# Performance work log

Measured on AMD Instinct MI355X. Metric: run time of the kernel, lower is better.

The kernel has to match this reference:

```python
import jax, jax.numpy as jnp
import numpy as np

VOCAB, EMBED, HIDDEN, LAYERS = 128, 256, 512, 2
B, T = 64, 512


def setup_inputs() -> dict:
    key = jax.random.key(0)
    ks = jax.random.split(key, 10)
    x = jax.random.randint(ks[0], (B, T), 0, VOCAB)
    emb = jax.random.normal(ks[1], (VOCAB, EMBED), jnp.float32) * 0.02
    emb = emb.at[0].set(0.0)  # padding_idx=0
    inp = {"x": x, "embedding": emb}
    in_dims = [EMBED, HIDDEN]
    for l in range(LAYERS):
        s = 1.0 / np.sqrt(in_dims[l])
        inp[f"W_xh{l}"] = jax.random.uniform(ks[2 + 3 * l], (HIDDEN, in_dims[l]), jnp.float32, -s, s)
        # orthogonal-ish init for W_hh
        a = jax.random.normal(ks[3 + 3 * l], (HIDDEN, HIDDEN), jnp.float32)
        q, _ = jnp.linalg.qr(a)
        inp[f"W_hh{l}"] = q
        inp[f"b_h{l}"] = jnp.zeros((HIDDEN,), jnp.float32)
    s = 1.0 / np.sqrt(HIDDEN)
    inp["W_hy"] = jax.random.uniform(ks[8], (VOCAB, HIDDEN), jnp.float32, -s, s)
    inp["b_y"] = jax.random.uniform(ks[9], (VOCAB,), jnp.float32, -s, s)
    return inp


def _rnn_layer(layer_in, W_xh, W_hh, b_h):
    # layer_in: (B, T, D). Precompute input projection for all t, scan recurrence.
    xW = jnp.einsum('btd,hd->bth', layer_in, W_xh) + b_h  # (B, T, H)
    h0 = jnp.zeros((layer_in.shape[0], W_hh.shape[0]), layer_in.dtype)

    def step(h_prev, xW_t):
        h_t = jnp.tanh(xW_t + h_prev @ W_hh.T)
        return h_t, h_t

    h_last, hs = jax.lax.scan(step, h0, jnp.swapaxes(xW, 0, 1))  # hs: (T, B, H)
    return jnp.swapaxes(hs, 0, 1), h_last


def reference(x, embedding, W_xh0, W_hh0, b_h0, W_xh1, W_hh1, b_h1, W_hy, b_y):
    layer_in = embedding[x]  # (B, T, E)
    hidden = []
    for W_xh, W_hh, b_h in ((W_xh0, W_hh0, b_h0), (W_xh1, W_hh1, b_h1)):
        layer_in, h_last = _rnn_layer(layer_in, W_xh, W_hh, b_h)
        hidden.append(h_last)
    logits = jnp.einsum('bth,vh->btv', layer_in, W_hy) + b_y
    return (logits, *hidden)
```

## Files before the change

### kernel.cpp

```cpp
#include <hip/hip_runtime.h>
#include <hip/hip_fp16.h>

typedef _Float16 f16x8 __attribute__((ext_vector_type(8)));
typedef float f32x4 __attribute__((ext_vector_type(4)));
typedef unsigned int u32x4 __attribute__((ext_vector_type(4)));
typedef unsigned int u32x2 __attribute__((ext_vector_type(2)));
typedef unsigned long long u64;

static constexpr int T_SEQ = 512;
static constexpr int BATCH = 64;
static constexpr int HID   = 512;
static constexpr int VOC   = 128;

static constexpr int AOFF_EMB  = 0;
static constexpr int AOFF_WXH0 = 32768;
static constexpr int AOFF_WHH0 = 163840;
static constexpr int AOFF_WXH1 = 425984;
static constexpr int AOFF_WHH1 = 688128;
static constexpr int AOFF_WHY  = 950272;
static constexpr int ATOT      = 1015808;

static constexpr size_t OFF_RING   = 16384;
static constexpr size_t RING_BYTES = 32ull * 4 * 512 * 16;
static constexpr size_t OFF_HIST   = OFF_RING + RING_BYTES;
static constexpr size_t HIST_BYTES = 512ull * 16 * 512 * 16;
static constexpr size_t OFF_ARENA  = OFF_HIST + HIST_BYTES;
static constexpr size_t OFF_XW0    = OFF_ARENA + 2ull * ATOT;
static constexpr size_t PLANE_B    = (size_t)T_SEQ * BATCH * HID * 2;
static constexpr size_t OFF_H1A    = OFF_XW0 + PLANE_B;

__device__ __forceinline__ unsigned short h2u(_Float16 h) {
  union { _Float16 h; unsigned short u; } c; c.h = h; return c.u;
}
__device__ __forceinline__ _Float16 u2h(unsigned short u) {
  union { unsigned short u; _Float16 h; } c; c.u = u; return c.h;
}
__device__ __forceinline__ float fast_tanh(float x) {
  float e = __expf(2.0f * x);
  return 1.0f - 2.0f * __builtin_amdgcn_rcpf(e + 1.0f);
}

__device__ __forceinline__ void store16_sys(u64* addr, u64 data, unsigned tag) {
  u32x4 v;
  v.x = (unsigned)data; v.y = (unsigned)(data >> 32);
  v.z = tag;            v.w = 0u;
  asm volatile("global_store_dwordx4 %0, %1, off sc0 sc1"
               :: "v"(addr), "v"(v) : "memory");
}
__device__ __forceinline__ void issue3x16(const u64* a, const u64* b, const u64* c,
                                          u32x4& v0, u32x4& v1, u32x4& v2) {
  asm volatile("global_load_dwordx4 %0, %3, off sc0 sc1\n\t"
               "global_load_dwordx4 %1, %4, off sc0 sc1\n\t"
               "global_load_dwordx4 %2, %5, off sc0 sc1"
               : "=&v"(v0), "=&v"(v1), "=&v"(v2)
               : "v"(a), "v"(b), "v"(c)
               : "memory");
}
__device__ __forceinline__ void issue4x16(const u64* a, const u64* b, const u64* c,
                                          const u64* d, u32x4& v0, u32x4& v1,
                                          u32x4& v2, u32x4& v3) {
  asm volatile("global_load_dwordx4 %0, %4, off sc0 sc1\n\t"
               "global_load_dwordx4 %1, %5, off sc0 sc1\n\t"
               "global_load_dwordx4 %2, %6, off sc0 sc1\n\t"
               "global_load_dwordx4 %3, %7, off sc0 sc1"
               : "=&v"(v0), "=&v"(v1), "=&v"(v2), "=&v"(v3)
               : "v"(a), "v"(b), "v"(c), "v"(d)
               : "memory");
}
__device__ __forceinline__ void wait3(u32x4& v0, u32x4& v1, u32x4& v2) {
  asm volatile("s_waitcnt vmcnt(0)" : "+v"(v0), "+v"(v1), "+v"(v2) :: "memory");
}
__device__ __forceinline__ void wait4_v3(u32x4& v0, u32x4& v1, u32x4& v2, u32x4& v3) {
  asm volatile("s_waitcnt vmcnt(3)" : "+v"(v0), "+v"(v1), "+v"(v2), "+v"(v3) :: "memory");
}
__device__ __forceinline__ void wait4_v0(u32x4& v0, u32x4& v1, u32x4& v2, u32x4& v3) {
  asm volatile("s_waitcnt vmcnt(0)" : "+v"(v0), "+v"(v1), "+v"(v2), "+v"(v3) :: "memory");
}
__device__ __forceinline__ void load3x16_sys(const u64* a, const u64* b, const u64* c,
                                             u32x4& v0, u32x4& v1, u32x4& v2) {
  asm volatile("global_load_dwordx4 %0, %3, off sc0 sc1\n\t"
               "global_load_dwordx4 %1, %4, off sc0 sc1\n\t"
               "global_load_dwordx4 %2, %5, off sc0 sc1\n\t"
               "s_waitcnt vmcnt(0)"
               : "=&v"(v0), "=&v"(v1), "=&v"(v2)
               : "v"(a), "v"(b), "v"(c)
               : "memory");
}
__device__ __forceinline__ void load4x16_sys(const u64* a, const u64* b, const u64* c,
                                             const u64* d, u32x4& v0, u32x4& v1,
                                             u32x4& v2, u32x4& v3) {
  asm volatile("global_load_dwordx4 %0, %4, off sc0 sc1\n\t"
               "global_load_dwordx4 %1, %5, off sc0 sc1\n\t"
               "global_load_dwordx4 %2, %6, off sc0 sc1\n\t"
               "global_load_dwordx4 %3, %7, off sc0 sc1\n\t"
               "s_waitcnt vmcnt(0)"
               : "=&v"(v0), "=&v"(v1), "=&v"(v2), "=&v"(v3)
               : "v"(a), "v"(b), "v"(c), "v"(d)
               : "memory");
}

__global__ __launch_bounds__(256) void canon_kernel(
    const float* p0, const float* p1, const float* p2, const float* p3,
    const float* p4, const float* p5, _Float16* __restrict__ dst,
    int* __restrict__ ringhist) {
  const int NZ = (int)((RING_BYTES + HIST_BYTES) / 4);
  for (int i = blockIdx.x * 256 + threadIdx.x; i < NZ; i += gridDim.x * 256)
    ringhist[i] = 0;
  const float* srcs[6] = {p0, p1, p2, p3, p4, p5};
  const int ns[6] = {32768, 131072, 262144, 262144, 262144, 65536};
  for (int i = blockIdx.x * 256 + threadIdx.x; i < ATOT; i += gridDim.x * 256) {
    int off = i, s = 0;
    while (off >= ns[s]) { off -= ns[s]; ++s; }
    dst[i] = (_Float16)srcs[s][off];
  }
}

__global__ __launch_bounds__(256) void xw0_kernel(
    const int* __restrict__ x, const _Float16* __restrict__ emb,
    const _Float16* __restrict__ Wxh, const float* __restrict__ bh,
    _Float16* __restrict__ xwf) {
  __shared__ _Float16 Bs[64][264];
  const int t = blockIdx.x, n0 = blockIdx.y * 64, tid = threadIdx.x;
#pragma unroll
  for (int rep = 0; rep < 8; ++rep) {
    int flat = rep * 256 + tid;
    int row = flat >> 5, c8 = flat & 31;
    *(f16x8*)&Bs[row][c8 * 8] = *(const f16x8*)&Wxh[(size_t)(n0 + row) * 256 + c8 * 8];
  }
  __syncthreads();
  const int wv = tid >> 6, lane = tid & 63, l15 = lane & 15, quad = lane >> 4;
  const int b = wv * 16 + l15;
  const int idx = x[b * 512 + t];
  f32x4 acc[4];
#pragma unroll
  for (int nt = 0; nt < 4; ++nt) { float bv = bh[n0 + nt * 16 + l15]; acc[nt] = {bv, bv, bv, bv}; }
#pragma unroll
  for (int kc = 0; kc < 8; ++kc) {
    f16x8 a = *(const f16x8*)&emb[(size_t)idx * 256 + kc * 32 + quad * 8];
#pragma unroll
    for (int nt = 0; nt < 4; ++nt) {
      f16x8 bf = *(const f16x8*)&Bs[nt * 16 + l15][kc * 32 + quad * 8];
      acc[nt] = __builtin_amdgcn_mfma_f32_16x16x32_f16(a, bf, acc[nt], 0, 0, 0);
    }
  }
#pragma unroll
  for (int nt = 0; nt < 4; ++nt) {
    unsigned int lo = (unsigned int)h2u((_Float16)acc[nt][0]) |
                      ((unsigned int)h2u((_Float16)acc[nt][1]) << 16);
    unsigned int hi = (unsigned int)h2u((_Float16)acc[nt][2]) |
                      ((unsigned int)h2u((_Float16)acc[nt][3]) << 16);
    u32x2 pk = {lo, hi};
    *(u32x2*)&xwf[(size_t)t * 32768 + (size_t)(n0 + nt * 16 + l15) * 64 + wv * 16 + quad * 4] = pk;
  }
}

__device__ __forceinline__ void layer0_loop(
    const _Float16* __restrict__ Whh, const _Float16* __restrict__ xwf,
    u64* __restrict__ hist, _Float16* alds, const int g, const int q, const int tid) {
  u64* aldsu = (u64*)alds;
  const int lane = tid & 63, wv = tid >> 6, l15 = lane & 15, quad = lane >> 4;
  const int n0 = q * 128 + wv * 16;

  u32x4 Bw[16];
#pragma unroll
  for (int i = 0; i < 16; ++i) {
    const int kc = (q * 4 + i) & 15;
    Bw[i] = *(const u32x4*)&Whh[(size_t)(n0 + l15) * 512 + kc * 32 + quad * 8];
  }

  int pquar[3];
  {
    int pi = 0;
    for (int qq = 0; qq < 4; ++qq)
      if (qq != q) pquar[pi++] = qq;
  }

  const _Float16* xwb = xwf + (size_t)(n0 + l15) * 64 + g * 16 + quad * 4;
  u32x2 pfx = *(const u32x2*)xwb;

  for (int t = 0; t < T_SEQ; ++t) {
#pragma unroll
    for (int i = 0; i < 16; ++i) asm volatile("" : "+v"(Bw[i]));

    f32x4 accA, accB = {0.f, 0.f, 0.f, 0.f};
    accA[0] = (float)u2h((unsigned short)(pfx.x & 0xFFFFu));
    accA[1] = (float)u2h((unsigned short)(pfx.x >> 16));
    accA[2] = (float)u2h((unsigned short)(pfx.y & 0xFFFFu));
    accA[3] = (float)u2h((unsigned short)(pfx.y >> 16));
    if (t + 1 < T_SEQ) pfx = *(const u32x2*)(xwb + (size_t)(t + 1) * 32768);

    if (t > 0) {
      const u64* a0 = hist + (((size_t)(t - 1) * 16 + g * 4 + pquar[0]) * 512 + tid) * 2;
      const u64* a1 = hist + (((size_t)(t - 1) * 16 + g * 4 + pquar[1]) * 512 + tid) * 2;
      const u64* a2 = hist + (((size_t)(t - 1) * 16 + g * 4 + pquar[2]) * 512 + tid) * 2;
      u32x4 r0, r1, r2;
      issue3x16(a0, a1, a2, r0, r1, r2);

#pragma unroll
      for (int i = 0; i < 4; ++i) {
        const int kc = q * 4 + i;
        f16x8 a = *(const f16x8*)&alds[kc * 512 + lane * 8];
        accA = __builtin_amdgcn_mfma_f32_16x16x32_f16(
            a, __builtin_bit_cast(f16x8, Bw[i]), accA, 0, 0, 0);
      }

      wait3(r0, r1, r2);
      const unsigned wtag = (unsigned)t;
      while ((r0.z != wtag) | (r1.z != wtag) | (r2.z != wtag))
        load3x16_sys(a0, a1, a2, r0, r1, r2);

      aldsu[pquar[0] * 512 + tid] = ((u64)r0.y << 32) | r0.x;
      aldsu[pquar[1] * 512 + tid] = ((u64)r1.y << 32) | r1.x;
      aldsu[pquar[2] * 512 + tid] = ((u64)r2.y << 32) | r2.x;
      __syncthreads();

#pragma unroll
      for (int i = 4; i < 16; ++i) {
        const int kc = (q * 4 + i) & 15;
        f16x8 a = *(const f16x8*)&alds[kc * 512 + lane * 8];
        if (i & 1)
          accB = __builtin_amdgcn_mfma_f32_16x16x32_f16(
              a, __builtin_bit_cast(f16x8, Bw[i]), accB, 0, 0, 0);
        else
          accA = __builtin_amdgcn_mfma_f32_16x16x32_f16(
              a, __builtin_bit_cast(f16x8, Bw[i]), accA, 0, 0, 0);
      }
      __syncthreads();
    }

    {
      f32x4 s = accA + accB;
      const int n = n0 + l15;
      const int kc = n >> 5, qd = (n >> 3) & 3, j = n & 7;
#pragma unroll
      for (int r = 0; r < 4; ++r)
        alds[kc * 512 + (qd * 16 + quad * 4 + r) * 8 + j] = (_Float16)fast_tanh(s[r]);
    }
    asm volatile("s_waitcnt lgkmcnt(0)" ::: "memory");
    __builtin_amdgcn_sched_barrier(0);
    {
      u64 msg = aldsu[q * 512 + tid];
      store16_sys(hist + (((size_t)t * 16 + g * 4 + q) * 512 + tid) * 2,
                  msg, (unsigned)(t + 1));
    }
    __syncthreads();
  }
}

__device__ __forceinline__ void layer1_loop(
    const _Float16* __restrict__ Whh, const _Float16* __restrict__ Wxh,
    const float* __restrict__ bh, const u64* __restrict__ hist,
    u64* __restrict__ ring, _Float16* __restrict__ h1A,
    _Float16* alds, _Float16* xlds, const int g, const int q, const int tid) {
  u64* aldsu = (u64*)alds;
  u64* xldsu = (u64*)xlds;
  const int lane = tid & 63, wv = tid >> 6, l15 = lane & 15, quad = lane >> 4;
  const int n0 = q * 128 + wv * 16;

  u32x4 Bh[16], Bx[16];
#pragma unroll
  for (int i = 0; i < 16; ++i) {
    const int kc = (q * 4 + i) & 15;
    Bh[i] = *(const u32x4*)&Whh[(size_t)(n0 + l15) * 512 + kc * 32 + quad * 8];
  }
#pragma unroll
  for (int i = 0; i < 16; ++i)
    Bx[i] = *(const u32x4*)&Wxh[(size_t)(n0 + l15) * 512 + i * 32 + quad * 8];
  const float bv = bh[n0 + l15];

  u64* pring[3];
  int pquar[3];
  {
    int pi = 0;
    for (int qq = 0; qq < 4; ++qq)
      if (qq != q) { pring[pi] = ring + (size_t)(16 + g * 4 + qq) * 4096; pquar[pi] = qq; ++pi; }
  }
  u64* myring = ring + (size_t)(16 + g * 4 + q) * 4096;

  for (int u = 0; u < T_SEQ; ++u) {
#pragma unroll
    for (int i = 0; i < 16; ++i) asm volatile("" : "+v"(Bh[i]));
#pragma unroll
    for (int i = 0; i < 16; ++i) asm volatile("" : "+v"(Bx[i]));

    f32x4 accA = {bv, bv, bv, bv};
    f32x4 accB = {0.f, 0.f, 0.f, 0.f}, accC = {0.f, 0.f, 0.f, 0.f},
          accD = {0.f, 0.f, 0.f, 0.f};
    const unsigned htag = (unsigned)(u + 1);

    const u64* hb = hist + ((size_t)(u * 16 + g * 4) * 512 + tid) * 2;
    const u64* h0a = hb, *h1a = hb + 1024, *h2a = hb + 2048, *h3a = hb + 3072;
    const int slot = (u - 1) & 3;
    const u64* a0 = pring[0] + (size_t)slot * 1024 + tid * 2;
    const u64* a1 = pring[1] + (size_t)slot * 1024 + tid * 2;
    const u64* a2 = pring[2] + (size_t)slot * 1024 + tid * 2;
    u32x4 hv0, hv1, hv2, hv3, r0, r1, r2;

    issue4x16(h0a, h1a, h2a, h3a, hv0, hv1, hv2, hv3);
    if (u > 0) {
      issue3x16(a0, a1, a2, r0, r1, r2);
#pragma unroll
      for (int i = 0; i < 4; ++i) {
        const int kc = q * 4 + i;
        f16x8 a = *(const f16x8*)&alds[kc * 512 + lane * 8];
        accA = __builtin_amdgcn_mfma_f32_16x16x32_f16(
            a, __builtin_bit_cast(f16x8, Bh[i]), accA, 0, 0, 0);
      }
      wait4_v3(hv0, hv1, hv2, hv3);
    } else {
      wait4_v0(hv0, hv1, hv2, hv3);
    }
    if (__any((hv0.z != htag) | (hv1.z != htag) | (hv2.z != htag) | (hv3.z != htag))) {
      do {
        load4x16_sys(h0a, h1a, h2a, h3a, hv0, hv1, hv2, hv3);
      } while (__any((hv0.z != htag) | (hv1.z != htag) |
                     (hv2.z != htag) | (hv3.z != htag)));
      if (u > 0) issue3x16(a0, a1, a2, r0, r1, r2);
    }
    xldsu[0 * 512 + tid] = ((u64)hv0.y << 32) | hv0.x;
    xldsu[1 * 512 + tid] = ((u64)hv1.y << 32) | hv1.x;
    xldsu[2 * 512 + tid] = ((u64)hv2.y << 32) | hv2.x;
    xldsu[3 * 512 + tid] = ((u64)hv3.y << 32) | hv3.x;
    __syncthreads();

#pragma unroll
    for (int kc = 0; kc < 16; ++kc) {
      f16x8 a = *(const f16x8*)&xlds[kc * 512 + lane * 8];
      if (kc < 8)
        accB = __builtin_amdgcn_mfma_f32_16x16x32_f16(
            a, __builtin_bit_cast(f16x8, Bx[kc]), accB, 0, 0, 0);
      else
        accC = __builtin_amdgcn_mfma_f32_16x16x32_f16(
            a, __builtin_bit_cast(f16x8, Bx[kc]), accC, 0, 0, 0);
    }

    if (u > 0) {
      const unsigned wtag = (unsigned)u;
      wait3(r0, r1, r2);
      while ((r0.z != wtag) | (r1.z != wtag) | (r2.z != wtag))
        load3x16_sys(a0, a1, a2, r0, r1, r2);

      if (q == 0) {
        u64* dplane = (u64*)h1A + ((size_t)(u - 1) * 4 + g) * 2048;
        dplane[pquar[0] * 512 + tid] = ((u64)r0.y << 32) | r0.x;
        dplane[pquar[1] * 512 + tid] = ((u64)r1.y << 32) | r1.x;
        dplane[pquar[2] * 512 + tid] = ((u64)r2.y << 32) | r2.x;
      }
      aldsu[pquar[0] * 512 + tid] = ((u64)r0.y << 32) | r0.x;
      aldsu[pquar[1] * 512 + tid] = ((u64)r1.y << 32) | r1.x;
      aldsu[pquar[2] * 512 + tid] = ((u64)r2.y << 32) | r2.x;
      __syncthreads();

#pragma unroll
      for (int i = 4; i < 16; ++i) {
        const int kc = (q * 4 + i) & 15;
        f16x8 a = *(const f16x8*)&alds[kc * 512 + lane * 8];
        if (i & 1)
          accD = __builtin_amdgcn_mfma_f32_16x16x32_f16(
              a, __builtin_bit_cast(f16x8, Bh[i]), accD, 0, 0, 0);
        else
          accA = __builtin_amdgcn_mfma_f32_16x16x32_f16(
              a, __builtin_bit_cast(f16x8, Bh[i]), accA, 0, 0, 0);
      }
    }
    __syncthreads();
    {
      f32x4 s = (accA + accD) + (accB + accC);
      const int n = n0 + l15;
      const int kc = n >> 5, qd = (n >> 3) & 3, j = n & 7;
#pragma unroll
      for (int r = 0; r < 4; ++r)
        alds[kc * 512 + (qd * 16 + quad * 4 + r) * 8 + j] = (_Float16)fast_tanh(s[r]);
    }
    asm volatile("s_waitcnt lgkmcnt(0)" ::: "memory");
    __builtin_amdgcn_sched_barrier(0);
    {
      u64 msg = aldsu[q * 512 + tid];
      store16_sys(myring + (size_t)(u & 3) * 1024 + tid * 2, msg, (unsigned)(u + 1));
      if (q == 0)
        ((u64*)h1A)[((size_t)u * 4 + g) * 2048 + tid] = msg;
    }
    __syncthreads();
  }

  if (q == 0) {
    const int slot = (T_SEQ - 1) & 3;
    const u64* a0 = pring[0] + (size_t)slot * 1024 + tid * 2;
    const u64* a1 = pring[1] + (size_t)slot * 1024 + tid * 2;
    const u64* a2 = pring[2] + (size_t)slot * 1024 + tid * 2;
    u32x4 r0, r1, r2;
    load3x16_sys(a0, a1, a2, r0, r1, r2);
    const unsigned wtag = (unsigned)T_SEQ;
    while ((r0.z != wtag) | (r1.z != wtag) | (r2.z != wtag))
      load3x16_sys(a0, a1, a2, r0, r1, r2);
    u64* dplane = (u64*)h1A + ((size_t)(T_SEQ - 1) * 4 + g) * 2048;
    dplane[pquar[0] * 512 + tid] = ((u64)r0.y << 32) | r0.x;
    dplane[pquar[1] * 512 + tid] = ((u64)r1.y << 32) | r1.x;
    dplane[pquar[2] * 512 + tid] = ((u64)r2.y << 32) | r2.x;
  }
}

__global__ __launch_bounds__(512, 1) void rnn_fused_kernel(
    const _Float16* __restrict__ Whh0, const _Float16* __restrict__ xwf0,
    const _Float16* __restrict__ Whh1, const _Float16* __restrict__ Wxh1,
    const float* __restrict__ bh1,
    u64* __restrict__ ring, u64* __restrict__ hist, _Float16* __restrict__ h1A) {
  __shared__ _Float16 lds[32 * 512];
  const int bid = blockIdx.x, tid = threadIdx.x;
  if (bid < 16) {
    layer0_loop(Whh0, xwf0, hist, lds, bid & 3, bid >> 2, tid);
  } else {
    const int b = bid - 16;
    layer1_loop(Whh1, Wxh1, bh1, hist, ring, h1A, lds, lds + 16 * 512,
                b & 3, b >> 2, tid);
  }
}

__global__ __launch_bounds__(256) void logits_kernel(
    const _Float16* __restrict__ h1A, const _Float16* __restrict__ Why,
    const float* __restrict__ by, float* __restrict__ out) {
  const int t = blockIdx.x;
  const int wv = threadIdx.x >> 6, lane = threadIdx.x & 63;
  const int l15 = lane & 15, quad = lane >> 4, bb = wv * 16;
  f32x4 acc[8];
#pragma unroll
  for (int vt = 0; vt < 8; ++vt) { float bvv = by[vt * 16 + l15]; acc[vt] = {bvv, bvv, bvv, bvv}; }
#pragma unroll
  for (int kc = 0; kc < 16; ++kc) {
    f16x8 a = *(const f16x8*)&h1A[(((size_t)t * 4 + wv) * 16 + kc) * 512 + lane * 8];
#pragma unroll
    for (int vt = 0; vt < 8; ++vt) {
      f16x8 b = *(const f16x8*)&Why[(size_t)(vt * 16 + l15) * 512 + kc * 32 + quad * 8];
      acc[vt] = __builtin_amdgcn_mfma_f32_16x16x32_f16(a, b, acc[vt], 0, 0, 0);
    }
  }
#pragma unroll
  for (int vt = 0; vt < 8; ++vt)
#pragma unroll
    for (int r = 0; r < 4; ++r)
      out[((size_t)(bb + quad * 4 + r) * 512 + t) * 128 + vt * 16 + l15] = acc[vt][r];
}

__global__ void hlast_kernel(const u64* __restrict__ hist,
                             const _Float16* __restrict__ h1A,
                             float* __restrict__ out) {
  const size_t LOG = (size_t)BATCH * T_SEQ * VOC;
  const size_t HL = (size_t)BATCH * HID;
  int tid = blockIdx.x * 256 + threadIdx.x;
  if (tid < (int)HL) {
    const int b = tid >> 9, n = tid & 511;
    const int gg = b >> 4, m = b & 15;
    const int kc = n >> 5, qd = (n >> 3) & 3, j = n & 7;
    const int pf = kc * 512 + (qd * 16 + m) * 8 + j;
    const int p = pf >> 2;
    const u64 d = hist[(((size_t)(T_SEQ - 1) * 16 + gg * 4 + (p >> 9)) * 512 + (p & 511)) * 2];
    out[LOG + tid] = (float)u2h((unsigned short)(d >> ((pf & 3) * 16)));
    const size_t idx = (((size_t)(T_SEQ - 1) * 4 + gg) * 16 + kc) * 512 + (qd * 16 + m) * 8 + j;
    out[LOG + HL + tid] = (float)h1A[idx];
  }
}

extern "C" void kernel_launch(void* const* d_in, const int* in_sizes, int n_in,
                              void* d_out, int out_size, void* d_ws, size_t ws_size,
                              hipStream_t stream) {
  const int* x = (const int*)d_in[0];
  float* out = (float*)d_out;
  char* ws = (char*)d_ws;
  u64* ring = (u64*)(ws + OFF_RING);
  u64* hist = (u64*)(ws + OFF_HIST);
  _Float16* arena = (_Float16*)(ws + OFF_ARENA);
  _Float16* xw0f = (_Float16*)(ws + OFF_XW0);
  _Float16* h1A  = (_Float16*)(ws + OFF_H1A);

  canon_kernel<<<512, 256, 0, stream>>>(
      (const float*)d_in[1], (const float*)d_in[2], (const float*)d_in[3],
      (const float*)d_in[5], (const float*)d_in[6], (const float*)d_in[8],
      arena, (int*)ring);

  xw0_kernel<<<dim3(512, 8), 256, 0, stream>>>(
      x, arena + AOFF_EMB, arena + AOFF_WXH0, (const float*)d_in[4], xw0f);

  rnn_fused_kernel<<<32, 512, 0, stream>>>(
      arena + AOFF_WHH0, xw0f,
      arena + AOFF_WHH1, arena + AOFF_WXH1, (const float*)d_in[7],
      ring, hist, h1A);

  logits_kernel<<<512, 256, 0, stream>>>(
      h1A, arena + AOFF_WHY, (const float*)d_in[9], out);

  hlast_kernel<<<(BATCH * HID + 255) / 256, 256, 0, stream>>>(hist, h1A, out);
}
```

Before: 1.198 ms.

## Prefetch next-step layer-0 hidden input into double-buffered LDS in layer-1 loop

The layer-1 recurrence now loads layer-0's h for step u+1 during step u and stages it into a second LDS buffer. The x-projection MFMAs therefore read already-staged data instead of waiting on a cross-block poll at the start of every step. The ring loads for peer quarters are issued first, and the h1A history stores are moved after the MFMAs, so global stores overlap compute. This costs more LDS (the buffer grows) and more complex vmcnt bookkeeping, with some risk of ordering mistakes in the waitcnt counts.

```diff
diff --git a/kernel.cpp b/kernel.cpp
--- a/kernel.cpp
+++ b/kernel.cpp
@@ -70,11 +70,14 @@
 __device__ __forceinline__ void wait3(u32x4& v0, u32x4& v1, u32x4& v2) {
   asm volatile("s_waitcnt vmcnt(0)" : "+v"(v0), "+v"(v1), "+v"(v2) :: "memory");
 }
-__device__ __forceinline__ void wait4_v3(u32x4& v0, u32x4& v1, u32x4& v2, u32x4& v3) {
-  asm volatile("s_waitcnt vmcnt(3)" : "+v"(v0), "+v"(v1), "+v"(v2), "+v"(v3) :: "memory");
-}
-__device__ __forceinline__ void wait4_v0(u32x4& v0, u32x4& v1, u32x4& v2, u32x4& v3) {
-  asm volatile("s_waitcnt vmcnt(0)" : "+v"(v0), "+v"(v1), "+v"(v2), "+v"(v3) :: "memory");
+__device__ __forceinline__ void wait3_v4(u32x4& v0, u32x4& v1, u32x4& v2) {
+  asm volatile("s_waitcnt vmcnt(4)" : "+v"(v0), "+v"(v1), "+v"(v2) :: "memory");
+}
+__device__ __forceinline__ void wait4_v1(u32x4& v0, u32x4& v1, u32x4& v2, u32x4& v3) {
+  asm volatile("s_waitcnt vmcnt(1)" : "+v"(v0), "+v"(v1), "+v"(v2), "+v"(v3) :: "memory");
+}
+__device__ __forceinline__ void drain_all() {
+  asm volatile("s_waitcnt vmcnt(0)" ::: "memory");
 }
 __device__ __forceinline__ void load3x16_sys(const u64* a, const u64* b, const u64* c,
                                              u32x4& v0, u32x4& v1, u32x4& v2) {
@@ -277,6 +280,20 @@
   }
   u64* myring = ring + (size_t)(16 + g * 4 + q) * 4096;
 
+  {
+    const u64* hb = hist + ((size_t)(g * 4) * 512 + tid) * 2;
+    u32x4 hv0, hv1, hv2, hv3;
+    load4x16_sys(hb, hb + 1024, hb + 2048, hb + 3072, hv0, hv1, hv2, hv3);
+    while (__any((hv0.z != 1u) | (hv1.z != 1u) | (hv2.z != 1u) | (hv3.z != 1u)))
+      load4x16_sys(hb, hb + 1024, hb + 2048, hb + 3072, hv0, hv1, hv2, hv3);
+    xldsu[0 * 512 + tid] = ((u64)hv0.y << 32) | hv0.x;
+    xldsu[1 * 512 + tid] = ((u64)hv1.y << 32) | hv1.x;
+    xldsu[2 * 512 + tid] = ((u64)hv2.y << 32) | hv2.x;
+    xldsu[3 * 512 + tid] = ((u64)hv3.y << 32) | hv3.x;
+  }
+  __syncthreads();
+
+  int cur = 0;
   for (int u = 0; u < T_SEQ; ++u) {
 #pragma unroll
     for (int i = 0; i < 16; ++i) asm volatile("" : "+v"(Bh[i]));
@@ -286,19 +303,20 @@
     f32x4 accA = {bv, bv, bv, bv};
     f32x4 accB = {0.f, 0.f, 0.f, 0.f}, accC = {0.f, 0.f, 0.f, 0.f},
           accD = {0.f, 0.f, 0.f, 0.f};
-    const unsigned htag = (unsigned)(u + 1);
-
-    const u64* hb = hist + ((size_t)(u * 16 + g * 4) * 512 + tid) * 2;
-    const u64* h0a = hb, *h1a = hb + 1024, *h2a = hb + 2048, *h3a = hb + 3072;
+
     const int slot = (u - 1) & 3;
     const u64* a0 = pring[0] + (size_t)slot * 1024 + tid * 2;
     const u64* a1 = pring[1] + (size_t)slot * 1024 + tid * 2;
     const u64* a2 = pring[2] + (size_t)slot * 1024 + tid * 2;
-    u32x4 hv0, hv1, hv2, hv3, r0, r1, r2;
-
-    issue4x16(h0a, h1a, h2a, h3a, hv0, hv1, hv2, hv3);
+    u32x4 r0, r1, r2, hv0, hv1, hv2, hv3;
+
+    if (u > 0) issue3x16(a0, a1, a2, r0, r1, r2);
+
+    const int un = (u + 1 < T_SEQ) ? (u + 1) : (T_SEQ - 1);
+    const u64* hb = hist + ((size_t)(un * 16 + g * 4) * 512 + tid) * 2;
+    issue4x16(hb, hb + 1024, hb + 2048, hb + 3072, hv0, hv1, hv2, hv3);
+
     if (u > 0) {
-      issue3x16(a0, a1, a2, r0, r1, r2);
 #pragma unroll
       for (int i = 0; i < 4; ++i) {
         const int kc = q * 4 + i;
@@ -306,49 +324,33 @@
         accA = __builtin_amdgcn_mfma_f32_16x16x32_f16(
             a, __builtin_bit_cast(f16x8, Bh[i]), accA, 0, 0, 0);
       }
-      wait4_v3(hv0, hv1, hv2, hv3);
-    } else {
-      wait4_v0(hv0, hv1, hv2, hv3);
-    }
-    if (__any((hv0.z != htag) | (hv1.z != htag) | (hv2.z != htag) | (hv3.z != htag))) {
-      do {
-        load4x16_sys(h0a, h1a, h2a, h3a, hv0, hv1, hv2, hv3);
-      } while (__any((hv0.z != htag) | (hv1.z != htag) |
-                     (hv2.z != htag) | (hv3.z != htag)));
-      if (u > 0) issue3x16(a0, a1, a2, r0, r1, r2);
-    }
-    xldsu[0 * 512 + tid] = ((u64)hv0.y << 32) | hv0.x;
-    xldsu[1 * 512 + tid] = ((u64)hv1.y << 32) | hv1.x;
-    xldsu[2 * 512 + tid] = ((u64)hv2.y << 32) | hv2.x;
-    xldsu[3 * 512 + tid] = ((u64)hv3.y << 32) | hv3.x;
-    __syncthreads();
-
-#pragma unroll
-    for (int kc = 0; kc < 16; ++kc) {
-      f16x8 a = *(const f16x8*)&xlds[kc * 512 + lane * 8];
-      if (kc < 8)
-        accB = __builtin_amdgcn_mfma_f32_16x16x32_f16(
-            a, __builtin_bit_cast(f16x8, Bx[kc]), accB, 0, 0, 0);
-      else
-        accC = __builtin_amdgcn_mfma_f32_16x16x32_f16(
-            a, __builtin_bit_cast(f16x8, Bx[kc]), accC, 0, 0, 0);
-    }
-
+    }
+    {
+      const _Float16* xb = xlds + cur * 8192;
+#pragma unroll
+      for (int kc = 0; kc < 16; ++kc) {
+        f16x8 a = *(const f16x8*)&xb[kc * 512 + lane * 8];
+        if (kc < 8)
+          accB = __builtin_amdgcn_mfma_f32_16x16x32_f16(
+              a, __builtin_bit_cast(f16x8, Bx[kc]), accB, 0, 0, 0);
+        else
+          accC = __builtin_amdgcn_mfma_f32_16x16x32_f16(
+              a, __builtin_bit_cast(f16x8, Bx[kc]), accC, 0, 0, 0);
+      }
+    }
+
+    u64 v0 = 0, v1 = 0, v2 = 0;
     if (u > 0) {
+      wait3_v4(r0, r1, r2);
       const unsigned wtag = (unsigned)u;
-      wait3(r0, r1, r2);
       while ((r0.z != wtag) | (r1.z != wtag) | (r2.z != wtag))
         load3x16_sys(a0, a1, a2, r0, r1, r2);
-
-      if (q == 0) {
-        u64* dplane = (u64*)h1A + ((size_t)(u - 1) * 4 + g) * 2048;
-        dplane[pquar[0] * 512 + tid] = ((u64)r0.y << 32) | r0.x;
-        dplane[pquar[1] * 512 + tid] = ((u64)r1.y << 32) | r1.x;
-        dplane[pquar[2] * 512 + tid] = ((u64)r2.y << 32) | r2.x;
-      }
-      aldsu[pquar[0] * 512 + tid] = ((u64)r0.y << 32) | r0.x;
-      aldsu[pquar[1] * 512 + tid] = ((u64)r1.y << 32) | r1.x;
-      aldsu[pquar[2] * 512 + tid] = ((u64)r2.y << 32) | r2.x;
+      v0 = ((u64)r0.y << 32) | r0.x;
+      v1 = ((u64)r1.y << 32) | r1.x;
+      v2 = ((u64)r2.y << 32) | r2.x;
+      aldsu[pquar[0] * 512 + tid] = v0;
+      aldsu[pquar[1] * 512 + tid] = v1;
+      aldsu[pquar[2] * 512 + tid] = v2;
       __syncthreads();
 
 #pragma unroll
@@ -362,8 +364,15 @@
           accA = __builtin_amdgcn_mfma_f32_16x16x32_f16(
               a, __builtin_bit_cast(f16x8, Bh[i]), accA, 0, 0, 0);
       }
+      if (q == 0) {
+        u64* dplane = (u64*)h1A + ((size_t)(u - 1) * 4 + g) * 2048;
+        dplane[pquar[0] * 512 + tid] = v0;
+        dplane[pquar[1] * 512 + tid] = v1;
+        dplane[pquar[2] * 512 + tid] = v2;
+      }
     }
     __syncthreads();
+    u64 msg;
     {
       f32x4 s = (accA + accD) + (accB + accC);
       const int n = n0 + l15;
@@ -374,14 +383,30 @@
     }
     asm volatile("s_waitcnt lgkmcnt(0)" ::: "memory");
     __builtin_amdgcn_sched_barrier(0);
-    {
-      u64 msg = aldsu[q * 512 + tid];
-      store16_sys(myring + (size_t)(u & 3) * 1024 + tid * 2, msg, (unsigned)(u + 1));
-      if (q == 0)
-        ((u64*)h1A)[((size_t)u * 4 + g) * 2048 + tid] = msg;
-    }
+    msg = aldsu[q * 512 + tid];
+    store16_sys(myring + (size_t)(u & 3) * 1024 + tid * 2, msg, (unsigned)(u + 1));
+
+    if (u + 1 < T_SEQ) {
+      wait4_v1(hv0, hv1, hv2, hv3);
+      const unsigned ht = (unsigned)(u + 2);
+      if (__any((hv0.z != ht) | (hv1.z != ht) | (hv2.z != ht) | (hv3.z != ht))) {
+        do {
+          load4x16_sys(hb, hb + 1024, hb + 2048, hb + 3072, hv0, hv1, hv2, hv3);
+        } while (__any((hv0.z != ht) | (hv1.z != ht) |
+                       (hv2.z != ht) | (hv3.z != ht)));
+      }
+      u64* xn = xldsu + (cur ^ 1) * 2048;
+      xn[0 * 512 + tid] = ((u64)hv0.y << 32) | hv0.x;
+      xn[1 * 512 + tid] = ((u64)hv1.y << 32) | hv1.x;
+      xn[2 * 512 + tid] = ((u64)hv2.y << 32) | hv2.x;
+      xn[3 * 512 + tid] = ((u64)hv3.y << 32) | hv3.x;
+    }
+    if (q == 0)
+      ((u64*)h1A)[((size_t)u * 4 + g) * 2048 + tid] = msg;
     __syncthreads();
-  }
+    cur ^= 1;
+  }
+  drain_all();
 
   if (q == 0) {
     const int slot = (T_SEQ - 1) & 3;
@@ -405,13 +430,13 @@
     const _Float16* __restrict__ Whh1, const _Float16* __restrict__ Wxh1,
     const float* __restrict__ bh1,
     u64* __restrict__ ring, u64* __restrict__ hist, _Float16* __restrict__ h1A) {
-  __shared__ _Float16 lds[32 * 512];
+  __shared__ _Float16 lds[24576];
   const int bid = blockIdx.x, tid = threadIdx.x;
   if (bid < 16) {
     layer0_loop(Whh0, xwf0, hist, lds, bid & 3, bid >> 2, tid);
   } else {
     const int b = bid - 16;
-    layer1_loop(Whh1, Wxh1, bh1, hist, ring, h1A, lds, lds + 16 * 512,
+    layer1_loop(Whh1, Wxh1, bh1, hist, ring, h1A, lds, lds + 8192,
                 b & 3, b >> 2, tid);
   }
 }
```

Measured after the change: 1.217 ms. About the same (+1.6%).
